# Optimization experiments

Hardware: AMD Instinct MI355X
Metric: run time of the kernel (lower is better)

Reference implementation:

```python
import jax, jax.numpy as jnp
import numpy as np

N_SRC = 100000
N_DST = 100000
N_EDGES = 1600000
IN_FEATS = 256
HEADS = 4
D_OUT = 64
NEG_SLOPE = 0.2


def setup_inputs() -> dict:
    key = jax.random.key(0)
    ks = jax.random.split(key, 7)
    return {
        "feat_src": jax.random.normal(ks[0], (N_SRC, IN_FEATS), dtype=jnp.float32),
        "feat_dst": jax.random.normal(ks[1], (N_DST, IN_FEATS), dtype=jnp.float32),
        "edge_src": jax.random.randint(ks[2], (N_EDGES,), 0, N_SRC, dtype=jnp.int32),
        "edge_dst": jax.random.randint(ks[3], (N_EDGES,), 0, N_DST, dtype=jnp.int32),
        "W": jax.random.normal(ks[4], (IN_FEATS, HEADS * D_OUT), dtype=jnp.float32) * 0.06,
        "attn_l": jax.random.normal(ks[5], (HEADS, D_OUT), dtype=jnp.float32) * 0.1,
        "attn_r": jax.random.normal(ks[6], (HEADS, D_OUT), dtype=jnp.float32) * 0.1,
    }


def reference(feat_src, feat_dst, edge_src, edge_dst, W, attn_l, attn_r):
    # fc projection (no bias), reshape to [N, H, D]
    fsrc = (feat_src @ W).reshape(-1, HEADS, D_OUT)
    fdst = (feat_dst @ W).reshape(-1, HEADS, D_OUT)
    # per-node attention logits: el [N_src, H], er [N_dst, H]
    el = jnp.einsum('nhd,hd->nh', fsrc, attn_l)
    er = jnp.einsum('nhd,hd->nh', fdst, attn_r)
    # per-edge logit = leaky_relu(el[src] + er[dst]); original uses raw exp (no max-sub)
    e = el[edge_src] + er[edge_dst]                          # [E, H]
    e = jnp.where(e >= 0, e, NEG_SLOPE * e)
    s = jnp.exp(e)                                           # [E, H]
    # edge softmax denominator: segment sum over dst nodes
    out_sum = jax.ops.segment_sum(s, edge_dst, num_segments=N_DST)  # [N_dst, H]
    a = s / out_sum[edge_dst]                                # [E, H]
    # weighted neighbor aggregation: m = ft[src] * a, summed per dst
    m = fsrc[edge_src] * a[:, :, None]                       # [E, H, D]
    rst = jax.ops.segment_sum(m, edge_dst, num_segments=N_DST)      # [N_dst, H, D]
    return rst
```

## Files before the change

### kernel.cpp

```cpp
#include <hip/hip_runtime.h>
#include <hip/hip_bf16.h>
#include <math.h>

#define N_SRC   100000
#define N_DST   100000
#define N_EDGES 1600000
#define IN_F    256
#define HEADS   4
#define D_OUT   64
#define NHD     256
#define NEG_SLOPE 0.2f

typedef __attribute__((ext_vector_type(8))) short          bf16x8;
typedef __attribute__((ext_vector_type(8))) unsigned short u16x8;
typedef __attribute__((ext_vector_type(4))) float          f32x4;

__device__ inline void split_bf16(float x, unsigned short& h, unsigned short& l) {
    unsigned u = __float_as_uint(x);
    unsigned uh = u + (0x7fffu + ((u >> 16) & 1u));
    h = (unsigned short)(uh >> 16);
    float hf = __uint_as_float(uh & 0xffff0000u);
    float r = x - hf;
    unsigned ur = __float_as_uint(r);
    l = (unsigned short)((ur + (0x7fffu + ((ur >> 16) & 1u))) >> 16);
}

__global__ void k_wr(const float* __restrict__ W, const float* __restrict__ ar,
                     float* __restrict__ wr) {
    __shared__ float a[NHD];
    int t = threadIdx.x;
    a[t] = ar[t];
    __syncthreads();
    float s[HEADS] = {0.f, 0.f, 0.f, 0.f};
    for (int h = 0; h < HEADS; ++h) {
        float acc = 0.f;
        #pragma unroll 8
        for (int d = 0; d < D_OUT; ++d)
            acc += W[t * NHD + h * D_OUT + d] * a[h * D_OUT + d];
        s[h] = acc;
    }
    *(float4*)&wr[t * 4] = make_float4(s[0], s[1], s[2], s[3]);
}

__global__ void k_wcast(const float* __restrict__ W,
                        unsigned short* __restrict__ Wht,
                        unsigned short* __restrict__ Wlt) {
    int n = blockIdx.x;
    int k = threadIdx.x;
    float x = W[k * NHD + n];
    unsigned short h, l;
    split_bf16(x, h, l);
    Wht[n * IN_F + k] = h;
    Wlt[n * IN_F + k] = l;
}

__global__ __launch_bounds__(256) void k_er(const float* __restrict__ fdst,
                                            const float* __restrict__ wr,
                                            float* __restrict__ er) {
    __shared__ float4 wrs[256];
    int t = threadIdx.x;
    wrs[t] = ((const float4*)wr)[t];
    __syncthreads();
    int node = blockIdx.x * 4 + (t >> 6);
    int lane = t & 63;
    float4 f = *(const float4*)&fdst[(size_t)node * IN_F + lane * 4];
    float4 w0 = wrs[lane * 4 + 0], w1 = wrs[lane * 4 + 1];
    float4 w2 = wrs[lane * 4 + 2], w3 = wrs[lane * 4 + 3];
    float px = f.x * w0.x + f.y * w1.x + f.z * w2.x + f.w * w3.x;
    float py = f.x * w0.y + f.y * w1.y + f.z * w2.y + f.w * w3.y;
    float pz = f.x * w0.z + f.y * w1.z + f.z * w2.z + f.w * w3.z;
    float pw = f.x * w0.w + f.y * w1.w + f.z * w2.w + f.w * w3.w;
    #pragma unroll
    for (int m = 1; m < 64; m <<= 1) {
        px += __shfl_xor(px, m);
        py += __shfl_xor(py, m);
        pz += __shfl_xor(pz, m);
        pw += __shfl_xor(pw, m);
    }
    if (lane == 0)
        *(float4*)&er[node * 4] = make_float4(px, py, pz, pw);
}

#define GBM 128
#define GBK 32
__global__ __launch_bounds__(512, 2) void k_gemm_mfma(
        const float* __restrict__ A, const unsigned short* __restrict__ Bht,
        const unsigned short* __restrict__ Blt, const float* __restrict__ al_g,
        float* __restrict__ C, float* __restrict__ el) {
    __shared__ __align__(16) unsigned short Ah[GBM][GBK], Al[GBM][GBK];
    __shared__ __align__(16) unsigned short Bh[NHD][GBK], Bl[NHD][GBK];
    const int t = threadIdx.x;
    const int m0 = blockIdx.x * GBM;
    const int wid = t >> 6, lane = t & 63;
    const int wm = wid >> 2, wn = wid & 3;
    const int fr = lane & 15, fq = lane >> 4;
    const int kb = fq * 8;

    f32x4 acc[4][4];
    #pragma unroll
    for (int m = 0; m < 4; ++m)
        #pragma unroll
        for (int n = 0; n < 4; ++n)
            acc[m][n] = (f32x4){0.f, 0.f, 0.f, 0.f};

    const int ar = t >> 2, ac = (t & 3) * 8;
    const bool avalid = (m0 + ar) < N_SRC;
    const float* aptr = A + (size_t)(m0 + ar) * IN_F + ac;
    const int bn = t >> 1, bk = (t & 1) * 16;

    for (int k0 = 0; k0 < IN_F; k0 += GBK) {
        float4 v0 = make_float4(0.f, 0.f, 0.f, 0.f), v1 = v0;
        if (avalid) {
            v0 = *(const float4*)(aptr + k0);
            v1 = *(const float4*)(aptr + k0 + 4);
        }
        u16x8 bh0 = *(const u16x8*)(Bht + (size_t)bn * IN_F + k0 + bk);
        u16x8 bh1 = *(const u16x8*)(Bht + (size_t)bn * IN_F + k0 + bk + 8);
        u16x8 bl0 = *(const u16x8*)(Blt + (size_t)bn * IN_F + k0 + bk);
        u16x8 bl1 = *(const u16x8*)(Blt + (size_t)bn * IN_F + k0 + bk + 8);
        float xs[8] = {v0.x, v0.y, v0.z, v0.w, v1.x, v1.y, v1.z, v1.w};
        u16x8 hv, lv;
        #pragma unroll
        for (int j = 0; j < 8; ++j) {
            unsigned short hh, ll;
            split_bf16(xs[j], hh, ll);
            hv[j] = hh; lv[j] = ll;
        }
        __syncthreads();
        *(u16x8*)&Ah[ar][ac] = hv;
        *(u16x8*)&Al[ar][ac] = lv;
        *(u16x8*)&Bh[bn][bk]     = bh0;
        *(u16x8*)&Bh[bn][bk + 8] = bh1;
        *(u16x8*)&Bl[bn][bk]     = bl0;
        *(u16x8*)&Bl[bn][bk + 8] = bl1;
        __syncthreads();
        bf16x8 afh[4], afl[4], bfh[4], bfl[4];
        #pragma unroll
        for (int m = 0; m < 4; ++m) {
            afh[m] = *(const bf16x8*)&Ah[wm * 64 + m * 16 + fr][kb];
            afl[m] = *(const bf16x8*)&Al[wm * 64 + m * 16 + fr][kb];
        }
        #pragma unroll
        for (int n = 0; n < 4; ++n) {
            bfh[n] = *(const bf16x8*)&Bh[wn * 64 + n * 16 + fr][kb];
            bfl[n] = *(const bf16x8*)&Bl[wn * 64 + n * 16 + fr][kb];
        }
        #pragma unroll
        for (int m = 0; m < 4; ++m)
            #pragma unroll
            for (int n = 0; n < 4; ++n) {
                acc[m][n] = __builtin_amdgcn_mfma_f32_16x16x32_bf16(afh[m], bfh[n], acc[m][n], 0, 0, 0);
                acc[m][n] = __builtin_amdgcn_mfma_f32_16x16x32_bf16(afh[m], bfl[n], acc[m][n], 0, 0, 0);
                acc[m][n] = __builtin_amdgcn_mfma_f32_16x16x32_bf16(afl[m], bfh[n], acc[m][n], 0, 0, 0);
            }
    }

    float alw[4];
    #pragma unroll
    for (int n = 0; n < 4; ++n) alw[n] = al_g[wn * 64 + n * 16 + fr];
    #pragma unroll
    for (int m = 0; m < 4; ++m) {
        int rbase = m0 + wm * 64 + m * 16 + fq * 4;
        float elp[4] = {0.f, 0.f, 0.f, 0.f};
        #pragma unroll
        for (int n = 0; n < 4; ++n) {
            f32x4 a = acc[m][n];
            int col = wn * 64 + n * 16 + fr;
            float w = alw[n];
            elp[0] += a[0] * w; elp[1] += a[1] * w;
            elp[2] += a[2] * w; elp[3] += a[3] * w;
            #pragma unroll
            for (int j = 0; j < 4; ++j)
                if (rbase + j < N_SRC)
                    C[(size_t)(rbase + j) * NHD + col] = a[j];
        }
        #pragma unroll
        for (int j = 0; j < 4; ++j) {
            float s = elp[j];
            s += __shfl_xor(s, 1); s += __shfl_xor(s, 2);
            s += __shfl_xor(s, 4); s += __shfl_xor(s, 8);
            if (fr == 0 && rbase + j < N_SRC)
                el[(rbase + j) * HEADS + wn] = s;
        }
    }
}

__global__ void k_hist(const int* __restrict__ edst, int* __restrict__ deg) {
    int e = blockIdx.x * 256 + threadIdx.x;
    if (e < N_EDGES) atomicAdd(&deg[edst[e]], 1);
}

#define SCAN_B 1024
__global__ __launch_bounds__(SCAN_B) void k_scanA(const int* __restrict__ deg,
                                                  int* __restrict__ off,
                                                  int* __restrict__ bsum) {
    int t = threadIdx.x, b = blockIdx.x;
    int i = b * SCAN_B + t;
    int v = (i < N_DST) ? deg[i] : 0;
    int incl = v;
    int lane = t & 63, w = t >> 6;
    #pragma unroll
    for (int d = 1; d < 64; d <<= 1) {
        int u = __shfl_up(incl, d);
        if (lane >= d) incl += u;
    }
    __shared__ int ws[16];
    if (lane == 63) ws[w] = incl;
    __syncthreads();
    if (t == 0) {
        int run = 0;
        for (int j = 0; j < 16; ++j) { int x = ws[j]; ws[j] = run; run += x; }
        bsum[b] = run;
    }
    __syncthreads();
    if (i < N_DST) off[i] = incl - v + ws[w];
}

__global__ void k_scanB(int* __restrict__ bsum, int nb) {
    if (threadIdx.x == 0 && blockIdx.x == 0) {
        int run = 0;
        for (int j = 0; j < nb; ++j) { int x = bsum[j]; bsum[j] = run; run += x; }
    }
}

__global__ __launch_bounds__(SCAN_B) void k_scanC(int* __restrict__ off,
                                                  const int* __restrict__ bsum) {
    int t = threadIdx.x, b = blockIdx.x;
    int i = b * SCAN_B + t;
    if (i < N_DST) off[i] += bsum[b];
    if (i == 0) off[N_DST] = N_EDGES;
}

__global__ void k_scatter(const int* __restrict__ esrc, const int* __restrict__ edst,
                          const int* __restrict__ off, int* __restrict__ cursor,
                          int* __restrict__ ssrc) {
    int e = blockIdx.x * 256 + threadIdx.x;
    if (e >= N_EDGES) return;
    int src = esrc[e], dst = edst[e];
    int pos = off[dst] + atomicAdd(&cursor[dst], 1);
    ssrc[pos] = src;
}

__global__ __launch_bounds__(256) void k_denom(const int* __restrict__ off,
                                               const int* __restrict__ ssrc,
                                               const float* __restrict__ el,
                                               const float* __restrict__ er,
                                               float* __restrict__ inv_den) {
    int n = blockIdx.x * 4 + (threadIdx.x >> 6);
    int lane = threadIdx.x & 63;
    int s0 = off[n], s1 = off[n + 1];
    float4 r4 = *(const float4*)&er[n * 4];
    float4 p = make_float4(0.f, 0.f, 0.f, 0.f);
    for (int i = s0 + lane; i < s1; i += 64) {
        int src = ssrc[i];
        float4 l4 = *(const float4*)&el[src * 4];
        float ex = l4.x + r4.x, ey = l4.y + r4.y;
        float ez = l4.z + r4.z, ew = l4.w + r4.w;
        ex = (ex >= 0.f) ? ex : NEG_SLOPE * ex;
        ey = (ey >= 0.f) ? ey : NEG_SLOPE * ey;
        ez = (ez >= 0.f) ? ez : NEG_SLOPE * ez;
        ew = (ew >= 0.f) ? ew : NEG_SLOPE * ew;
        p.x += __expf(ex); p.y += __expf(ey);
        p.z += __expf(ez); p.w += __expf(ew);
    }
    #pragma unroll
    for (int m = 1; m < 64; m <<= 1) {
        p.x += __shfl_xor(p.x, m);
        p.y += __shfl_xor(p.y, m);
        p.z += __shfl_xor(p.z, m);
        p.w += __shfl_xor(p.w, m);
    }
    if (lane == 0) {
        float4 inv;
        inv.x = (p.x > 0.f) ? 1.0f / p.x : 0.f;
        inv.y = (p.y > 0.f) ? 1.0f / p.y : 0.f;
        inv.z = (p.z > 0.f) ? 1.0f / p.z : 0.f;
        inv.w = (p.w > 0.f) ? 1.0f / p.w : 0.f;
        *(float4*)&inv_den[n * 4] = inv;
    }
}

__global__ __launch_bounds__(256) void k_agg(const int* __restrict__ off,
                                             const int* __restrict__ ssrc,
                                             const float* __restrict__ el,
                                             const float* __restrict__ er,
                                             const float* __restrict__ inv_den,
                                             const float* __restrict__ fsrc,
                                             float* __restrict__ out, int p) {
    int b = blockIdx.x;
    int t = threadIdx.x;
    int s0 = off[b], s1 = off[b + 1];
    int ws = t >> 5;
    int sl = t & 31;
    int c  = p * 128 + sl * 4;
    int h  = c >> 6;
    float erh = er[b * 4 + h];

    __shared__ float red[8][128];

    float4 acc = make_float4(0.f, 0.f, 0.f, 0.f);
    int i = s0 + ws;
    for (; i + 8 < s1; i += 16) {
        int srcA = ssrc[i], srcB = ssrc[i + 8];
        float eA = el[srcA * 4 + h] + erh;
        float eB = el[srcB * 4 + h] + erh;
        eA = (eA >= 0.f) ? eA : NEG_SLOPE * eA;
        eB = (eB >= 0.f) ? eB : NEG_SLOPE * eB;
        float aA = __expf(eA), aB = __expf(eB);
        float4 fA = *(const float4*)&fsrc[(size_t)srcA * NHD + c];
        float4 fB = *(const float4*)&fsrc[(size_t)srcB * NHD + c];
        acc.x += aA * fA.x; acc.y += aA * fA.y;
        acc.z += aA * fA.z; acc.w += aA * fA.w;
        acc.x += aB * fB.x; acc.y += aB * fB.y;
        acc.z += aB * fB.z; acc.w += aB * fB.w;
    }
    if (i < s1) {
        int src = ssrc[i];
        float e = el[src * 4 + h] + erh;
        e = (e >= 0.f) ? e : NEG_SLOPE * e;
        float a = __expf(e);
        float4 f = *(const float4*)&fsrc[(size_t)src * NHD + c];
        acc.x += a * f.x; acc.y += a * f.y;
        acc.z += a * f.z; acc.w += a * f.w;
    }
    *(float4*)&red[ws][sl * 4] = acc;
    __syncthreads();

    if (t < 128) {
        float r = red[0][t] + red[1][t] + red[2][t] + red[3][t]
                + red[4][t] + red[5][t] + red[6][t] + red[7][t];
        int col = p * 128 + t;
        out[(size_t)b * NHD + col] = r * inv_den[b * 4 + (col >> 6)];
    }
}

extern "C" void kernel_launch(void* const* d_in, const int* in_sizes, int n_in,
                              void* d_out, int out_size, void* d_ws, size_t ws_size,
                              hipStream_t stream) {
    const float* feat_src = (const float*)d_in[0];
    const float* feat_dst = (const float*)d_in[1];
    const int*   edge_src = (const int*)d_in[2];
    const int*   edge_dst = (const int*)d_in[3];
    const float* W        = (const float*)d_in[4];
    const float* attn_l   = (const float*)d_in[5];
    const float* attn_r   = (const float*)d_in[6];
    float* out = (float*)d_out;

    char* base = (char*)d_ws;
    float* fsrc     = (float*)(base);
    unsigned short* Wht = (unsigned short*)(base + 102400000);
    unsigned short* Wlt = (unsigned short*)(base + 102400000 + 131072);
    float* inv_den  = (float*)(base + 103000000);
    float* el       = (float*)(base + 128000000);
    float* er       = (float*)(base + 129600000);
    float* wr       = (float*)(base + 131200000);
    int*   deg      = (int*)  (base + 131204096);
    int*   off      = (int*)  (base + 131604096);
    int*   cursor   = (int*)  (base + 132004112);
    int*   bsum     = (int*)  (base + 132404112);
    int*   ssrc     = (int*)  (base + 132404624);

    hipMemsetAsync(deg, 0, N_DST * sizeof(int), stream);
    hipMemsetAsync(cursor, 0, N_DST * sizeof(int), stream);

    k_wr<<<1, 256, 0, stream>>>(W, attn_r, wr);
    k_wcast<<<256, 256, 0, stream>>>(W, Wht, Wlt);
    k_er<<<N_DST / 4, 256, 0, stream>>>(feat_dst, wr, er);
    int gblocks = (N_SRC + GBM - 1) / GBM;
    k_gemm_mfma<<<gblocks, 512, 0, stream>>>(feat_src, Wht, Wlt, attn_l, fsrc, el);
    k_hist<<<(N_EDGES + 255) / 256, 256, 0, stream>>>(edge_dst, deg);
    int nb = (N_DST + SCAN_B - 1) / SCAN_B;
    k_scanA<<<nb, SCAN_B, 0, stream>>>(deg, off, bsum);
    k_scanB<<<1, 64, 0, stream>>>(bsum, nb);
    k_scanC<<<nb, SCAN_B, 0, stream>>>(off, bsum);
    k_scatter<<<(N_EDGES + 255) / 256, 256, 0, stream>>>(
        edge_src, edge_dst, off, cursor, ssrc);
    k_denom<<<N_DST / 4, 256, 0, stream>>>(off, ssrc, el, er, inv_den);
    k_agg<<<N_DST, 256, 0, stream>>>(off, ssrc, el, er, inv_den, fsrc, out, 0);
    k_agg<<<N_DST, 256, 0, stream>>>(off, ssrc, el, er, inv_den, fsrc, out, 1);
}
```

Measured before the change: 780.4 us.

## Merge two half-column aggregation passes into one full-row pass, pad GEMM LDS

The aggregation kernel previously ran twice, each pass covering 128 of the 256 output columns, so every pass re-read the CSR offsets, source indices, el values and the exp computation. Now each wavefront covers a full 256-float row per edge, 4 wavefronts stride over the edges, and one launch writes all columns with nontemporal stores. Separately, the GEMM shared-memory tiles get 8 shorts of padding per row to reduce LDS bank conflicts. The trade-off is fewer edges in flight per block (4 wavefronts instead of 8 edge slots), which may lower memory-level parallelism on high-degree nodes.

Measured after the change: 741.3 us. 1.05x faster.

```diff
diff --git a/kernel.cpp b/kernel.cpp
--- a/kernel.cpp
+++ b/kernel.cpp
@@ -83,12 +83,13 @@
 
 #define GBM 128
 #define GBK 32
+#define GPAD 8
 __global__ __launch_bounds__(512, 2) void k_gemm_mfma(
         const float* __restrict__ A, const unsigned short* __restrict__ Bht,
         const unsigned short* __restrict__ Blt, const float* __restrict__ al_g,
         float* __restrict__ C, float* __restrict__ el) {
-    __shared__ __align__(16) unsigned short Ah[GBM][GBK], Al[GBM][GBK];
-    __shared__ __align__(16) unsigned short Bh[NHD][GBK], Bl[NHD][GBK];
+    __shared__ __align__(16) unsigned short Ah[GBM][GBK + GPAD], Al[GBM][GBK + GPAD];
+    __shared__ __align__(16) unsigned short Bh[NHD][GBK + GPAD], Bl[NHD][GBK + GPAD];
     const int t = threadIdx.x;
     const int m0 = blockIdx.x * GBM;
     const int wid = t >> 6, lane = t & 63;
@@ -286,29 +287,28 @@
                                              const float* __restrict__ er,
                                              const float* __restrict__ inv_den,
                                              const float* __restrict__ fsrc,
-                                             float* __restrict__ out, int p) {
+                                             float* __restrict__ out) {
     int b = blockIdx.x;
     int t = threadIdx.x;
     int s0 = off[b], s1 = off[b + 1];
-    int ws = t >> 5;
-    int sl = t & 31;
-    int c  = p * 128 + sl * 4;
-    int h  = c >> 6;
+    int w = t >> 6, lane = t & 63;
+    int h = lane >> 4;
+    int col = lane << 2;
     float erh = er[b * 4 + h];
 
-    __shared__ float red[8][128];
+    __shared__ float red[4][NHD];
 
     float4 acc = make_float4(0.f, 0.f, 0.f, 0.f);
-    int i = s0 + ws;
-    for (; i + 8 < s1; i += 16) {
-        int srcA = ssrc[i], srcB = ssrc[i + 8];
+    int i = s0 + w;
+    for (; i + 4 < s1; i += 8) {
+        int srcA = ssrc[i], srcB = ssrc[i + 4];
         float eA = el[srcA * 4 + h] + erh;
         float eB = el[srcB * 4 + h] + erh;
         eA = (eA >= 0.f) ? eA : NEG_SLOPE * eA;
         eB = (eB >= 0.f) ? eB : NEG_SLOPE * eB;
         float aA = __expf(eA), aB = __expf(eB);
-        float4 fA = *(const float4*)&fsrc[(size_t)srcA * NHD + c];
-        float4 fB = *(const float4*)&fsrc[(size_t)srcB * NHD + c];
+        float4 fA = *(const float4*)&fsrc[(size_t)srcA * NHD + col];
+        float4 fB = *(const float4*)&fsrc[(size_t)srcB * NHD + col];
         acc.x += aA * fA.x; acc.y += aA * fA.y;
         acc.z += aA * fA.z; acc.w += aA * fA.w;
         acc.x += aB * fB.x; acc.y += aB * fB.y;
@@ -319,19 +319,16 @@
         float e = el[src * 4 + h] + erh;
         e = (e >= 0.f) ? e : NEG_SLOPE * e;
         float a = __expf(e);
-        float4 f = *(const float4*)&fsrc[(size_t)src * NHD + c];
+        float4 f = *(const float4*)&fsrc[(size_t)src * NHD + col];
         acc.x += a * f.x; acc.y += a * f.y;
         acc.z += a * f.z; acc.w += a * f.w;
     }
-    *(float4*)&red[ws][sl * 4] = acc;
-    __syncthreads();
-
-    if (t < 128) {
-        float r = red[0][t] + red[1][t] + red[2][t] + red[3][t]
-                + red[4][t] + red[5][t] + red[6][t] + red[7][t];
-        int col = p * 128 + t;
-        out[(size_t)b * NHD + col] = r * inv_den[b * 4 + (col >> 6)];
-    }
+    *(float4*)&red[w][col] = acc;
+    __syncthreads();
+
+    float r = red[0][t] + red[1][t] + red[2][t] + red[3][t];
+    __builtin_nontemporal_store(r * inv_den[b * 4 + (t >> 6)],
+                                &out[(size_t)b * NHD + t]);
 }
 
 extern "C" void kernel_launch(void* const* d_in, const int* in_sizes, int n_in,
@@ -376,6 +373,5 @@
     k_scatter<<<(N_EDGES + 255) / 256, 256, 0, stream>>>(
         edge_src, edge_dst, off, cursor, ssrc);
     k_denom<<<N_DST / 4, 256, 0, stream>>>(off, ssrc, el, er, inv_den);
-    k_agg<<<N_DST, 256, 0, stream>>>(off, ssrc, el, er, inv_den, fsrc, out, 0);
-    k_agg<<<N_DST, 256, 0, stream>>>(off, ssrc, el, er, inv_den, fsrc, out, 1);
-}
+    k_agg<<<N_DST, 256, 0, stream>>>(off, ssrc, el, er, inv_den, fsrc, out);
+}
```
